# Performance work log

Hardware: AMD Instinct MI355X
Metric: run time of the kernel (lower is better)

Reference implementation:

```python
import jax, jax.numpy as jnp
import numpy as np

N_HEAD = 4
GROUPS = 32
EPS = 1e-5


def _group_norm(x, w, b):
    B, C, H, W = x.shape
    g = x.reshape(B, GROUPS, C // GROUPS, H, W)
    mu = g.mean(axis=(2, 3, 4), keepdims=True)
    var = ((g - mu) ** 2).mean(axis=(2, 3, 4), keepdims=True)
    g = (g - mu) * jax.lax.rsqrt(var + EPS)
    return g.reshape(B, C, H, W) * w[None, :, None, None] + b[None, :, None, None]


def _l2norm(x):
    # F.normalize(x, dim=-1): x / max(||x||_2, 1e-12)
    n = jnp.sqrt(jnp.sum(x * x, axis=-1, keepdims=True))
    return x / jnp.maximum(n, 1e-12)


def _masked_softmax(attn, kk):
    # topk indices -> scatter 1s -> masked softmax (faithful to torch scatter_ path)
    idx = jax.lax.top_k(attn, kk)[1]                      # [B,H,c,kk]
    mask = jax.nn.one_hot(idx, attn.shape[-1], dtype=attn.dtype).sum(-2)  # [B,H,c,c]
    return jax.nn.softmax(jnp.where(mask > 0, attn, -jnp.inf), axis=-1)


def setup_inputs() -> dict:
    key = jax.random.key(0)
    ks = jax.random.split(key, 8)
    B, C, H, W = 4, 256, 128, 128
    x = jax.random.normal(ks[0], (B, C, H, W), jnp.float32)
    gn_w = 1.0 + 0.02 * jax.random.normal(ks[1], (C,), jnp.float32)
    gn_b = 0.02 * jax.random.normal(ks[2], (C,), jnp.float32)
    w_qkv = jax.random.normal(ks[3], (3 * C, C), jnp.float32) / np.sqrt(C).astype(np.float32)
    w_dw = jax.random.normal(ks[4], (3 * C, 1, 3, 3), jnp.float32) / 3.0
    w_out = jax.random.normal(ks[5], (C, C), jnp.float32) / np.sqrt(C).astype(np.float32)
    b_out = 0.01 * jax.random.normal(ks[6], (C,), jnp.float32)
    temperature = jnp.ones((N_HEAD, 1, 1), jnp.float32)
    attn_w = jnp.full((4,), 0.2, jnp.float32)  # attn1..attn4 combine weights
    return dict(x=x, gn_w=gn_w, gn_b=gn_b, w_qkv=w_qkv, w_dw=w_dw,
                w_out=w_out, b_out=b_out, temperature=temperature, attn_w=attn_w)


def reference(x, gn_w, gn_b, w_qkv, w_dw, w_out, b_out, temperature, attn_w):
    B, C, H, W = x.shape
    c = C // N_HEAD
    xn = _group_norm(x, gn_w, gn_b)
    # 1x1 conv (no bias)
    qkv = jnp.einsum('oi,bihw->bohw', w_qkv, xn)
    # 3x3 depthwise conv, padding=1, groups=3C, no bias
    qkv = jax.lax.conv_general_dilated(
        qkv, w_dw, window_strides=(1, 1), padding=((1, 1), (1, 1)),
        feature_group_count=3 * C,
        dimension_numbers=('NCHW', 'OIHW', 'NCHW'))
    q, k, v = jnp.split(qkv, 3, axis=1)
    # b (head c) h w -> b head c (h w)
    q = q.reshape(B, N_HEAD, c, H * W)
    k = k.reshape(B, N_HEAD, c, H * W)
    v = v.reshape(B, N_HEAD, c, H * W)
    q = _l2norm(q)
    k = _l2norm(k)
    # FFT cross-correlation attention (fftshift over ALL axes, as torch default)
    q_fft = jnp.fft.fftshift(jnp.fft.rfft2(q))   # [B,H,c,HW//2+1] complex
    k_fft = jnp.fft.fftshift(jnp.fft.rfft2(k))
    attn = jnp.einsum('bhcf,bhdf->bhcd', q_fft, k_fft) * temperature  # complex [B,H,c,c]
    attn = jnp.fft.irfft2(jnp.fft.ifftshift(attn), s=(c, c))          # real [B,H,c,c]
    ks_list = [c // 2, (c * 2) // 3, (c * 3) // 4, (c * 4) // 5]
    out = None
    for i, kk in enumerate(ks_list):
        a = _masked_softmax(attn, kk)
        o = jnp.einsum('bhcd,bhds->bhcs', a, v) * attn_w[i]
        out = o if out is None else out + o
    out = out.reshape(B, C, H, W)
    out = jnp.einsum('oi,bihw->bohw', w_out, out) + b_out[None, :, None, None]
    return out
```

## Files before the change

### kernel.cpp

```cpp
#include <hip/hip_runtime.h>
#include <math.h>

#define NC 256
#define CH3 768
#define HWSZ 16384

typedef __attribute__((ext_vector_type(8))) short short8;
typedef __attribute__((ext_vector_type(4))) float f32x4;
typedef __attribute__((ext_vector_type(4))) unsigned int u32x4;

static const size_t OFF_TW1   = 0;
static const size_t OFF_TW2   = 32768;
static const size_t OFF_HM    = 65536;
static const size_t OFF_SCALE = 65600;
static const size_t OFF_SHIFT = 66624;
static const size_t OFF_PACK  = 67648;
static const size_t OFF_AW    = 182336;
static const size_t OFF_GNP   = 444480;
static const size_t SHARED_END= 446528;

static const size_t R_QKV  = 0;
static const size_t R_SCR  = 12582912;
static const size_t R_H    = 25165824;
static const size_t R_PP   = 29360128;
static const size_t R_RP   = 30408704;
static const size_t R_ATTN = 31457280;
static const size_t R_ACOMB= 31473664;
static const size_t R_PS   = 31490048;
static const size_t R_RS   = 31506432;
static const size_t R_DWP  = 31522816;
static const size_t R_SSUM = 31532032;
static const size_t R_SALT = 31532800;
static const size_t R_SSQ  = 31533568;
static const size_t RSTRIDE= 31534336;
static const size_t UROFF  = 4194304;
static const size_t UIOFF  = 8388608;

#define TDA_RH 0
#define TDA_RL 8192
#define TDA_IH 16384
#define TDA_IL 24576
#define ETA_RH 32768
#define ETA_RL 40960
#define ETA_IH 49152
#define ETA_IL 57344
#define STB_RH 65536
#define STB_RL 73728
#define STB_IH 81920
#define STB_IL 90112
#define STB_NIH 98304
#define STB_NIL 106496

#define AWQ_H 0
#define AWQ_L 98304
#define AWO_H 196608
#define AWO_L 229376

__device__ inline unsigned short b16rn(float x){
  unsigned u = __float_as_uint(x);
  return (unsigned short)((u + 0x7FFFu + ((u>>16)&1u)) >> 16);
}
__device__ inline unsigned int pk_hi(float x, float y){
  return (__float_as_uint(x)>>16) | (__float_as_uint(y) & 0xFFFF0000u);
}
__device__ inline unsigned int pk_lo(float x, float y){
  float xl = x - __uint_as_float(__float_as_uint(x) & 0xFFFF0000u);
  float yl = y - __uint_as_float(__float_as_uint(y) & 0xFFFF0000u);
  return (unsigned)b16rn(xl) | ((unsigned)b16rn(yl)<<16);
}
__device__ inline short8 ld8g(const unsigned int* p){ return *(const short8*)p; }
__device__ inline short8 ld8s(const unsigned short* p){ return *(const short8*)p; }
__device__ inline void wr_split(unsigned short* H, unsigned short* L, size_t o, float v){
  unsigned u = __float_as_uint(v);
  H[o] = (unsigned short)(u >> 16);
  L[o] = b16rn(v - __uint_as_float(u & 0xFFFF0000u));
}

__global__ __launch_bounds__(256) void init_tables_k(float* __restrict__ ws){
  int idx = blockIdx.x*256 + threadIdx.x;
  float2* tw1 = (float2*)(ws + OFF_TW1);
  float2* tw2 = (float2*)(ws + OFF_TW2);
  unsigned int* pk = (unsigned int*)(ws + OFF_PACK);
  const double P2 = 6.283185307179586476925286766559005;
  int m = idx >> 7, k = idx & 127;
  double a2 = P2 * (double)(m*k) / 16384.0;
  tw1[idx] = make_float2((float)cos(a2), (float)(-sin(a2)));
  tw2[idx] = make_float2((float)cos(a2), (float)( sin(a2)));
  if (idx < 64){
    double acc = 0.0;
    for (int v = 1; v < 32; v++) acc += sin(P2 * (double)((v*idx) & 63) / 64.0);
    ws[OFF_HM + idx] = (float)(-acc / 32.0);
  }
  if (idx < 8192){
    int r = idx >> 6, kp = idx & 63;
    int k0 = 2*kp, k1 = 2*kp+1;
    double a0 = P2 * (double)((r*k0) & 127) / 128.0;
    double a1 = P2 * (double)((r*k1) & 127) / 128.0;
    float c0 = (float)cos(a0), c1 = (float)cos(a1);
    float s0 = (float)sin(a0), s1 = (float)sin(a1);
    pk[TDA_RH + idx] = pk_hi(c0, c1);  pk[TDA_RL + idx] = pk_lo(c0, c1);
    pk[TDA_IH + idx] = pk_hi(-s0,-s1); pk[TDA_IL + idx] = pk_lo(-s0,-s1);
    pk[ETA_RH + idx] = pk_hi(c0, c1);  pk[ETA_RL + idx] = pk_lo(c0, c1);
    pk[ETA_IH + idx] = pk_hi(s0, s1);  pk[ETA_IL + idx] = pk_lo(s0, s1);
    float sr0, si0, sr1, si1;
    {
      int d0 = (r - k0) & 127, d1 = (r - k1) & 127;
      if (d0 == 0){ sr0 = 64.f; si0 = 0.f; }
      else if ((d0 & 1) == 0){ sr0 = 0.f; si0 = 0.f; }
      else { double th = 3.1415926535897932384626 * (double)d0 / 128.0;
             sr0 = 1.f; si0 = (float)(cos(th)/sin(th)); }
      if (d1 == 0){ sr1 = 64.f; si1 = 0.f; }
      else if ((d1 & 1) == 0){ sr1 = 0.f; si1 = 0.f; }
      else { double th = 3.1415926535897932384626 * (double)d1 / 128.0;
             sr1 = 1.f; si1 = (float)(cos(th)/sin(th)); }
    }
    pk[STB_RH + idx]  = pk_hi(sr0, sr1);  pk[STB_RL + idx]  = pk_lo(sr0, sr1);
    pk[STB_IH + idx]  = pk_hi(si0, si1);  pk[STB_IL + idx]  = pk_lo(si0, si1);
    pk[STB_NIH + idx] = pk_hi(-si0,-si1); pk[STB_NIL + idx] = pk_lo(-si0,-si1);
  }
}

__global__ __launch_bounds__(256) void wpack_k(const float* __restrict__ wqkv, const float* __restrict__ wout,
                                               unsigned int* __restrict__ aw){
  int id = blockIdx.x*256 + threadIdx.x;
  int row = id >> 7, kp = id & 127;
  if (row < CH3){
    float v0 = wqkv[row*256 + 2*kp], v1 = wqkv[row*256 + 2*kp + 1];
    aw[AWQ_H + row*128 + kp] = pk_hi(v0, v1);
    aw[AWQ_L + row*128 + kp] = pk_lo(v0, v1);
  } else {
    int r2 = row - CH3;
    float v0 = wout[r2*256 + 2*kp], v1 = wout[r2*256 + 2*kp + 1];
    aw[AWO_H + r2*128 + kp] = pk_hi(v0, v1);
    aw[AWO_L + r2*128 + kp] = pk_lo(v0, v1);
  }
}

__global__ __launch_bounds__(256) void gn_part_k(const float* __restrict__ x, float2* __restrict__ part){
  int id = blockIdx.x;
  const float4* p = (const float4*)(x + (size_t)id*HWSZ);
  int tid = threadIdx.x;
  float s = 0.f, sq = 0.f;
  #pragma unroll
  for (int i = 0; i < 16; i++){
    float4 v = p[tid + i*256];
    s  += v.x+v.y+v.z+v.w;
    sq += v.x*v.x+v.y*v.y+v.z*v.z+v.w*v.w;
  }
  __shared__ float r1[256], r2[256];
  r1[tid]=s; r2[tid]=sq; __syncthreads();
  for (int off=128; off; off>>=1){
    if (tid<off){ r1[tid]+=r1[tid+off]; r2[tid]+=r2[tid+off]; }
    __syncthreads();
  }
  if (tid==0) part[id] = make_float2(r1[0], r2[0]);
}
__global__ __launch_bounds__(128) void gn_fin_k(const float2* __restrict__ part, const float* __restrict__ gw,
                                                const float* __restrict__ gb, float* __restrict__ scale,
                                                float* __restrict__ shift){
  int bg = threadIdx.x;
  int b = bg >> 5, g = bg & 31;
  float s = 0.f, sq = 0.f;
  #pragma unroll
  for (int i = 0; i < 8; i++){
    float2 v = part[b*NC + g*8 + i];
    s += v.x; sq += v.y;
  }
  const float n = 8.0f*HWSZ;
  float mu = s/n, var = sq/n - mu*mu;
  float rs = rsqrtf(var + 1e-5f);
  for (int i = 0; i < 8; i++){
    int ch = g*8 + i;
    float sc = rs * gw[ch];
    scale[b*NC + ch] = sc;
    shift[b*NC + ch] = gb[ch] - mu*sc;
  }
}

__global__ __launch_bounds__(256) void packx_k(const float* __restrict__ xbase, const float* __restrict__ scale,
                                               const float* __restrict__ shift, float* __restrict__ R0,
                                               size_t rstride){
  int bz = blockIdx.z;
  const float* xb = xbase + (size_t)bz*NC*HWSZ;
  const float* sc = scale + bz*NC;
  const float* sh = shift + bz*NC;
  unsigned int* BqH = (unsigned int*)(R0 + (size_t)bz*rstride + R_H);
  unsigned int* BqL = BqH + 2097152;
  int kb = blockIdx.y;
  int n = blockIdx.x*256 + threadIdx.x;
  float v[8];
  #pragma unroll
  for (int c = 0; c < 8; c++){
    int ch = kb*8 + c;
    v[c] = xb[(size_t)ch*HWSZ + n]*sc[ch] + sh[ch];
  }
  u32x4 h, l;
  #pragma unroll
  for (int q = 0; q < 4; q++){
    h[q] = pk_hi(v[2*q], v[2*q+1]);
    l[q] = pk_lo(v[2*q], v[2*q+1]);
  }
  *(u32x4*)&BqH[((size_t)kb*HWSZ + n)*4] = h;
  *(u32x4*)&BqL[((size_t)kb*HWSZ + n)*4] = l;
}

__global__ __launch_bounds__(256) void gemm_pk(const unsigned int* __restrict__ Ah, const unsigned int* __restrict__ Al,
                                               const unsigned int* __restrict__ Bh0, const unsigned int* __restrict__ Bl0,
                                               const float* __restrict__ bias, float* __restrict__ C0,
                                               size_t bstride, size_t cstride){
  const unsigned int* Bh = Bh0 + (size_t)blockIdx.z*bstride;
  const unsigned int* Bl = Bl0 + (size_t)blockIdx.z*bstride;
  float* C = C0 + (size_t)blockIdx.z*cstride;
  int tid = threadIdx.x;
  int lane = tid & 63, wid = tid >> 6;
  int m0 = blockIdx.y*128, n0 = blockIdx.x*128;
  int wr = (wid>>1)*64, wc = (wid&1)*64;
  int lr = lane & 15, lk = lane >> 4;
  f32x4 acc[4][4] = {};
  size_t aoff[4], boff[4];
  #pragma unroll
  for (int i=0;i<4;i++) aoff[i] = (size_t)(m0 + wr + i*16 + lr)*128 + lk*4;
  #pragma unroll
  for (int j=0;j<4;j++) boff[j] = ((size_t)lk*HWSZ + n0 + wc + j*16 + lr)*4;
  short8 aH[2][4], aL[2][4], bH[2][4], bL[2][4];
  #pragma unroll
  for (int i=0;i<4;i++){ aH[0][i] = ld8g(Ah + aoff[i]); aL[0][i] = ld8g(Al + aoff[i]); }
  #pragma unroll
  for (int j=0;j<4;j++){ bH[0][j] = ld8g(Bh + boff[j]); bL[0][j] = ld8g(Bl + boff[j]); }
  #pragma unroll
  for (int kt = 0; kt < 8; kt++){
    int cur = kt & 1, nxt = cur ^ 1;
    if (kt < 7){
      size_t da = (size_t)(kt+1)*16;
      size_t db = (size_t)(kt+1)*4*HWSZ*4;
      #pragma unroll
      for (int i=0;i<4;i++){ aH[nxt][i] = ld8g(Ah + aoff[i] + da); aL[nxt][i] = ld8g(Al + aoff[i] + da); }
      #pragma unroll
      for (int j=0;j<4;j++){ bH[nxt][j] = ld8g(Bh + boff[j] + db); bL[nxt][j] = ld8g(Bl + boff[j] + db); }
    }
    #pragma unroll
    for (int i=0;i<4;i++)
      #pragma unroll
      for (int j=0;j<4;j++){
        acc[i][j] = __builtin_amdgcn_mfma_f32_16x16x32_bf16(aH[cur][i], bH[cur][j], acc[i][j], 0,0,0);
        acc[i][j] = __builtin_amdgcn_mfma_f32_16x16x32_bf16(aH[cur][i], bL[cur][j], acc[i][j], 0,0,0);
        acc[i][j] = __builtin_amdgcn_mfma_f32_16x16x32_bf16(aL[cur][i], bH[cur][j], acc[i][j], 0,0,0);
      }
  }
  #pragma unroll
  for (int i=0;i<4;i++){
    #pragma unroll
    for (int e=0;e<4;e++){
      int row = m0 + wr + i*16 + lk*4 + e;
      float bb = bias ? bias[row] : 0.0f;
      #pragma unroll
      for (int j=0;j<4;j++)
        C[(size_t)row*HWSZ + n0 + wc + j*16 + lr] = acc[i][j][e] + bb;
    }
  }
}

__global__ __launch_bounds__(256) void dwconv_tiled_k(float* __restrict__ R0, size_t rstride,
                                                      const float* __restrict__ wdw){
  float* Rb = R0 + (size_t)blockIdx.y*rstride;
  int blk = blockIdx.x;
  int ch = blk >> 2, sl = blk & 3;
  int h0 = sl*32;
  const float* in = Rb + R_SCR + (size_t)ch*HWSZ;
  float* part = Rb + R_DWP;
  float w[9];
  #pragma unroll
  for (int i=0;i<9;i++) w[i] = wdw[ch*9+i];
  __shared__ float tile[34][132];
  __shared__ float r0[256], r1[256], r2[256];
  int tid = threadIdx.x;
  #pragma unroll
  for (int i = 0; i < 5; i++){
    int id = tid + i*256;
    if (id < 1088){
      int r = id >> 5, c4 = id & 31;
      int gh = h0 - 1 + r;
      float4 v = (gh >= 0 && gh < 128) ? *(const float4*)&in[gh*128 + c4*4]
                                       : make_float4(0.f,0.f,0.f,0.f);
      *(float4*)&tile[r][c4*4] = v;
    }
  }
  __syncthreads();
  float s=0.f, sa=0.f, sq=0.f;
  #pragma unroll
  for (int it=0; it<4; it++){
    int idx = it*256 + tid;
    int lh = idx >> 5;
    int xq = idx & 31;
    int xb4 = xq*4;
    float o[4];
    #pragma unroll
    for (int e=0;e<4;e++){
      int xw = xb4 + e;
      float acc = 0.f;
      #pragma unroll
      for (int ky=0; ky<3; ky++){
        const float* tr = &tile[lh+ky][xw];
        if (xw > 0)   acc += tr[-1]*w[ky*3+0];
                      acc += tr[ 0]*w[ky*3+1];
        if (xw < 127) acc += tr[ 1]*w[ky*3+2];
      }
      o[e] = acc;
      s += acc; sq += acc*acc;
      sa += (e & 1) ? -acc : acc;
    }
    int sbase = (h0+lh)*128 + xb4;
    if (ch < 256){
      unsigned short* QHo = (unsigned short*)(Rb + R_QKV);
      unsigned short* QLo = (unsigned short*)(Rb + R_QKV + 2097152);
      size_t ro = (size_t)ch*HWSZ;
      #pragma unroll
      for (int e=0;e<4;e++){
        int sf = (16384 - (sbase+e)) & 16383;
        wr_split(QHo, QLo, ro + sf, o[e]);
      }
    } else if (ch < 512){
      unsigned short* KHo = (unsigned short*)(Rb + R_H);
      unsigned short* KLo = (unsigned short*)(Rb + R_H + 2097152);
      size_t ro = (size_t)(ch-256)*HWSZ;
      #pragma unroll
      for (int e=0;e<4;e++)
        wr_split(KHo, KLo, ro + sbase+e, o[e]);
    } else {
      *(float4*)&(Rb + R_QKV + (size_t)ch*HWSZ)[sbase] = make_float4(o[0],o[1],o[2],o[3]);
    }
  }
  r0[tid]=s; r1[tid]=sa; r2[tid]=sq; __syncthreads();
  for (int off=128; off; off>>=1){
    if (tid<off){ r0[tid]+=r0[tid+off]; r1[tid]+=r1[tid+off]; r2[tid]+=r2[tid+off]; }
    __syncthreads();
  }
  if (tid==0){ part[blk]=r0[0]; part[3072+blk]=r1[0]; part[6144+blk]=r2[0]; }
}

__global__ __launch_bounds__(256) void fft1_mfma_k(const float* __restrict__ ws, float* __restrict__ R0,
                                                   size_t rstride){
  float* Rb = R0 + (size_t)blockIdx.y*rstride;
  const unsigned short* KH = (const unsigned short*)(Rb + R_H);
  const unsigned short* KL = (const unsigned short*)(Rb + R_H + 2097152);
  unsigned short* TRH = (unsigned short*)(Rb + R_SCR);
  unsigned short* TRL = TRH + 4194304;
  unsigned short* TIH = TRL + 4194304;
  unsigned short* TIL = TIH + 4194304;
  const unsigned int* PK = (const unsigned int*)(ws + OFF_PACK);
  const float2* tw1 = (const float2*)(ws + OFF_TW1);
  __shared__ unsigned int Bth[128][20], Btl[128][20];
  int tid = threadIdx.x;
  int lane = tid & 63, wid = tid >> 6;
  int wr = (wid>>1)*64, wc = (wid&1)*64;
  int lr = lane & 15, lk = lane >> 4;
  int row = blockIdx.x;
  f32x4 aR[4][4] = {}, aI[4][4] = {};
  int bc = tid & 127, grp = tid >> 7;
  for (int kt = 0; kt < 4; kt++){
    #pragma unroll
    for (int p=0;p<8;p++){
      int kp = grp*8 + p;
      int a = kt*32 + 2*kp;
      size_t o0 = (size_t)row*HWSZ + a*128 + bc;
      Bth[bc][kp] = (unsigned)KH[o0] | ((unsigned)KH[o0+128] << 16);
      Btl[bc][kp] = (unsigned)KL[o0] | ((unsigned)KL[o0+128] << 16);
    }
    __syncthreads();
    short8 bh[4], bl[4];
    #pragma unroll
    for (int j=0;j<4;j++){
      bh[j] = *(const short8*)&Bth[wc + j*16 + lr][lk*4];
      bl[j] = *(const short8*)&Btl[wc + j*16 + lr][lk*4];
    }
    #pragma unroll
    for (int i=0;i<4;i++){
      int off = (wr + i*16 + lr)*64 + kt*16 + lk*4;
      short8 ahR = ld8g(PK + TDA_RH + off), alR = ld8g(PK + TDA_RL + off);
      short8 ahI = ld8g(PK + TDA_IH + off), alI = ld8g(PK + TDA_IL + off);
      #pragma unroll
      for (int j=0;j<4;j++){
        aR[i][j] = __builtin_amdgcn_mfma_f32_16x16x32_bf16(ahR, bh[j], aR[i][j], 0,0,0);
        aR[i][j] = __builtin_amdgcn_mfma_f32_16x16x32_bf16(ahR, bl[j], aR[i][j], 0,0,0);
        aR[i][j] = __builtin_amdgcn_mfma_f32_16x16x32_bf16(alR, bh[j], aR[i][j], 0,0,0);
        aI[i][j] = __builtin_amdgcn_mfma_f32_16x16x32_bf16(ahI, bh[j], aI[i][j], 0,0,0);
        aI[i][j] = __builtin_amdgcn_mfma_f32_16x16x32_bf16(ahI, bl[j], aI[i][j], 0,0,0);
        aI[i][j] = __builtin_amdgcn_mfma_f32_16x16x32_bf16(alI, bh[j], aI[i][j], 0,0,0);
      }
    }
    __syncthreads();
  }
  #pragma unroll
  for (int i=0;i<4;i++)
    #pragma unroll
    for (int e=0;e<4;e++){
      int m = wr + i*16 + lk*4 + e;
      #pragma unroll
      for (int j=0;j<4;j++){
        int col = wc + j*16 + lr;
        float2 t = tw1[m*128 + col];
        float r = aR[i][j][e], im = aI[i][j][e];
        float vr = r*t.x - im*t.y, vi = r*t.y + im*t.x;
        size_t o = (size_t)m*32768 + row*128 + col;
        wr_split(TRH, TRL, o, vr);
        wr_split(TIH, TIL, o, vi);
      }
    }
}

__global__ __launch_bounds__(256) void fft2_mfma_k(const float* __restrict__ ws, float* __restrict__ R0,
                                                   size_t rstride){
  float* Rb = R0 + (size_t)blockIdx.y*rstride;
  const unsigned short* TRH = (const unsigned short*)(Rb + R_SCR);
  const unsigned short* TRL = TRH + 4194304;
  const unsigned short* TIH = TRL + 4194304;
  const unsigned short* TIL = TIH + 4194304;
  unsigned short* URH = (unsigned short*)(Rb + R_QKV + UROFF);
  unsigned short* URL = URH + 4194304;
  unsigned short* UIH = (unsigned short*)(Rb + R_SCR + UIOFF);
  unsigned short* UIL = UIH + 4194304;
  const unsigned int* PK = (const unsigned int*)(ws + OFF_PACK);
  const float2* tw2 = (const float2*)(ws + OFF_TW2);
  int tid = threadIdx.x, lane = tid & 63, wid = tid >> 6;
  int row = blockIdx.x >> 1, mh = blockIdx.x & 1;
  int wr = (wid>>1)*32, wc = (wid&1)*64;
  int lr = lane & 15, lk = lane >> 4;
  f32x4 aR[2][4] = {}, aI[2][4] = {};
  size_t aoff[2];
  #pragma unroll
  for (int i=0;i<2;i++) aoff[i] = (size_t)(mh*64 + wr + i*16 + lr)*32768 + row*128 + lk*8;
  #pragma unroll
  for (int kt = 0; kt < 4; kt++){
    short8 ahR[2], alR[2], ahI[2], alI[2];
    #pragma unroll
    for (int i=0;i<2;i++){
      size_t o = aoff[i] + kt*32;
      ahR[i] = ld8s(TRH + o); alR[i] = ld8s(TRL + o);
      ahI[i] = ld8s(TIH + o); alI[i] = ld8s(TIL + o);
    }
    #pragma unroll
    for (int j=0;j<4;j++){
      int boff = (wc + j*16 + lr)*64 + kt*16 + lk*4;
      short8 bhR = ld8g(PK + STB_RH + boff), blR = ld8g(PK + STB_RL + boff);
      short8 bhI = ld8g(PK + STB_IH + boff), blI = ld8g(PK + STB_IL + boff);
      short8 bhN = ld8g(PK + STB_NIH + boff), blN = ld8g(PK + STB_NIL + boff);
      #pragma unroll
      for (int i=0;i<2;i++){
        aR[i][j] = __builtin_amdgcn_mfma_f32_16x16x32_bf16(ahR[i], bhR, aR[i][j], 0,0,0);
        aR[i][j] = __builtin_amdgcn_mfma_f32_16x16x32_bf16(ahR[i], blR, aR[i][j], 0,0,0);
        aR[i][j] = __builtin_amdgcn_mfma_f32_16x16x32_bf16(alR[i], bhR, aR[i][j], 0,0,0);
        aR[i][j] = __builtin_amdgcn_mfma_f32_16x16x32_bf16(ahI[i], bhN, aR[i][j], 0,0,0);
        aR[i][j] = __builtin_amdgcn_mfma_f32_16x16x32_bf16(ahI[i], blN, aR[i][j], 0,0,0);
        aR[i][j] = __builtin_amdgcn_mfma_f32_16x16x32_bf16(alI[i], bhN, aR[i][j], 0,0,0);
        aI[i][j] = __builtin_amdgcn_mfma_f32_16x16x32_bf16(ahR[i], bhI, aI[i][j], 0,0,0);
        aI[i][j] = __builtin_amdgcn_mfma_f32_16x16x32_bf16(ahR[i], blI, aI[i][j], 0,0,0);
        aI[i][j] = __builtin_amdgcn_mfma_f32_16x16x32_bf16(alR[i], bhI, aI[i][j], 0,0,0);
        aI[i][j] = __builtin_amdgcn_mfma_f32_16x16x32_bf16(ahI[i], bhR, aI[i][j], 0,0,0);
        aI[i][j] = __builtin_amdgcn_mfma_f32_16x16x32_bf16(ahI[i], blR, aI[i][j], 0,0,0);
        aI[i][j] = __builtin_amdgcn_mfma_f32_16x16x32_bf16(alI[i], bhR, aI[i][j], 0,0,0);
      }
    }
  }
  #pragma unroll
  for (int i=0;i<2;i++){
    int f0b = mh*64 + wr + i*16 + lk*4;
    #pragma unroll
    for (int j=0;j<4;j++){
      int r = wc + j*16 + lr;
      unsigned long long prH=0ull, prL=0ull, piH=0ull, piL=0ull;
      #pragma unroll
      for (int e=0;e<4;e++){
        float2 t = tw2[(f0b+e)*128 + r];
        float rr = aR[i][j][e], ii = aI[i][j][e];
        float ur = rr*t.x - ii*t.y, ui = rr*t.y + ii*t.x;
        unsigned uur = __float_as_uint(ur), uui = __float_as_uint(ui);
        prH |= (unsigned long long)(uur >> 16) << (16*e);
        prL |= (unsigned long long)b16rn(ur - __uint_as_float(uur & 0xFFFF0000u)) << (16*e);
        piH |= (unsigned long long)(uui >> 16) << (16*e);
        piL |= (unsigned long long)b16rn(ui - __uint_as_float(uui & 0xFFFF0000u)) << (16*e);
      }
      size_t o = (size_t)row*HWSZ + r*128 + f0b;
      *(unsigned long long*)(URH + o) = prH;
      *(unsigned long long*)(URL + o) = prL;
      *(unsigned long long*)(UIH + o) = piH;
      *(unsigned long long*)(UIL + o) = piL;
    }
  }
}

__global__ __launch_bounds__(256) void fft3_mfma_k(const float* __restrict__ ws, float* __restrict__ R0,
                                                   size_t rstride){
  float* Rb = R0 + (size_t)blockIdx.y*rstride;
  const unsigned short* URH = (const unsigned short*)(Rb + R_QKV + UROFF);
  const unsigned short* URL = URH + 4194304;
  const unsigned short* UIH = (const unsigned short*)(Rb + R_SCR + UIOFF);
  const unsigned short* UIL = UIH + 4194304;
  unsigned short* HNH = (unsigned short*)(Rb + R_SCR);
  unsigned short* HNL = HNH + 4194304;
  const unsigned int* PK = (const unsigned int*)(ws + OFF_PACK);
  int tid = threadIdx.x, lane = tid & 63, wid = tid >> 6;
  int wr = (wid>>1)*64, wc = (wid&1)*64;
  int lr = lane & 15, lk = lane >> 4;
  int row = blockIdx.x;
  f32x4 ac[4][4] = {};
  size_t boff[4];
  #pragma unroll
  for (int j=0;j<4;j++) boff[j] = (size_t)row*HWSZ + (wc + j*16 + lr)*128 + lk*8;
  #pragma unroll
  for (int kt = 0; kt < 4; kt++){
    short8 bRh[4], bRl[4], bIh[4], bIl[4];
    #pragma unroll
    for (int j=0;j<4;j++){
      bRh[j] = ld8s(URH + boff[j] + kt*32);
      bRl[j] = ld8s(URL + boff[j] + kt*32);
      bIh[j] = ld8s(UIH + boff[j] + kt*32);
      bIl[j] = ld8s(UIL + boff[j] + kt*32);
    }
    #pragma unroll
    for (int i=0;i<4;i++){
      int off = (wr + i*16 + lr)*64 + kt*16 + lk*4;
      short8 ahR = ld8g(PK + ETA_RH + off), alR = ld8g(PK + ETA_RL + off);
      short8 ahI = ld8g(PK + ETA_IH + off), alI = ld8g(PK + ETA_IL + off);
      #pragma unroll
      for (int j=0;j<4;j++){
        ac[i][j] = __builtin_amdgcn_mfma_f32_16x16x32_bf16(ahR, bIh[j], ac[i][j], 0,0,0);
        ac[i][j] = __builtin_amdgcn_mfma_f32_16x16x32_bf16(ahR, bIl[j], ac[i][j], 0,0,0);
        ac[i][j] = __builtin_amdgcn_mfma_f32_16x16x32_bf16(alR, bIh[j], ac[i][j], 0,0,0);
        ac[i][j] = __builtin_amdgcn_mfma_f32_16x16x32_bf16(ahI, bRh[j], ac[i][j], 0,0,0);
        ac[i][j] = __builtin_amdgcn_mfma_f32_16x16x32_bf16(ahI, bRl[j], ac[i][j], 0,0,0);
        ac[i][j] = __builtin_amdgcn_mfma_f32_16x16x32_bf16(alI, bRh[j], ac[i][j], 0,0,0);
      }
    }
  }
  #pragma unroll
  for (int i=0;i<4;i++)
    #pragma unroll
    for (int e=0;e<4;e++){
      int m = wr + i*16 + lk*4 + e;
      #pragma unroll
      for (int j=0;j<4;j++){
        int col = wc + j*16 + lr;
        wr_split(HNH, HNL, (size_t)row*HWSZ + m*128 + col, ac[i][j][e]);
      }
    }
}

__global__ __launch_bounds__(256) void pri3_k(float* __restrict__ R0, size_t rstride){
  float* Rb = R0 + (size_t)blockIdx.z*rstride;
  int sp = blockIdx.x, head = blockIdx.y;
  const unsigned short* QH = (const unsigned short*)(Rb + R_QKV);
  const unsigned short* QL = (const unsigned short*)(Rb + R_QKV + 2097152);
  const unsigned short* KH = (const unsigned short*)(Rb + R_H);
  const unsigned short* KL = (const unsigned short*)(Rb + R_H + 2097152);
  const unsigned short* HNH = (const unsigned short*)(Rb + R_SCR);
  const unsigned short* HNL = HNH + 4194304;
  float* Pp = Rb + R_PP;
  float* Rp = Rb + R_RP;
  int tid = threadIdx.x, lane = tid & 63, wid = tid >> 6;
  int wr = (wid>>1)*32, wc = (wid&1)*32;
  int lr = lane & 15, lk = lane >> 4;
  size_t qoff[2], koff[2];
  #pragma unroll
  for (int i=0;i<2;i++) qoff[i] = (size_t)(head*64 + wr + i*16 + lr)*HWSZ + sp*256 + lk*8;
  #pragma unroll
  for (int j=0;j<2;j++) koff[j] = (size_t)(head*64 + wc + j*16 + lr)*HWSZ + sp*256 + lk*8;
  f32x4 aP[2][2] = {}, aRi[2][2] = {};
  short8 qh[2][2], ql[2][2], k1h[2][2], k1l[2][2], k2h[2][2], k2l[2][2];
#define LDPRI(B,T) { int d = (T)*32; \
    _Pragma("unroll") \
    for (int i=0;i<2;i++){ \
      qh[B][i] = ld8s(QH + qoff[i] + d); \
      ql[B][i] = ld8s(QL + qoff[i] + d); } \
    _Pragma("unroll") \
    for (int j=0;j<2;j++){ \
      k1h[B][j] = ld8s(KH + koff[j] + d); \
      k1l[B][j] = ld8s(KL + koff[j] + d); \
      k2h[B][j] = ld8s(HNH + koff[j] + d); \
      k2l[B][j] = ld8s(HNL + koff[j] + d); } }
  LDPRI(0,0);
  #pragma unroll
  for (int kt = 0; kt < 8; kt++){
    int cur = kt & 1;
    if (kt < 7) LDPRI(cur^1, kt+1);
    #pragma unroll
    for (int i=0;i<2;i++)
      #pragma unroll
      for (int j=0;j<2;j++){
        aP[i][j]  = __builtin_amdgcn_mfma_f32_16x16x32_bf16(qh[cur][i], k1h[cur][j], aP[i][j], 0,0,0);
        aP[i][j]  = __builtin_amdgcn_mfma_f32_16x16x32_bf16(qh[cur][i], k1l[cur][j], aP[i][j], 0,0,0);
        aP[i][j]  = __builtin_amdgcn_mfma_f32_16x16x32_bf16(ql[cur][i], k1h[cur][j], aP[i][j], 0,0,0);
        aRi[i][j] = __builtin_amdgcn_mfma_f32_16x16x32_bf16(qh[cur][i], k2h[cur][j], aRi[i][j], 0,0,0);
        aRi[i][j] = __builtin_amdgcn_mfma_f32_16x16x32_bf16(qh[cur][i], k2l[cur][j], aRi[i][j], 0,0,0);
        aRi[i][j] = __builtin_amdgcn_mfma_f32_16x16x32_bf16(ql[cur][i], k2h[cur][j], aRi[i][j], 0,0,0);
      }
  }
#undef LDPRI
  size_t obase = ((size_t)(sp*4 + head)) << 12;
  #pragma unroll
  for (int i=0;i<2;i++)
    #pragma unroll
    for (int e=0;e<4;e++){
      int row = wr + i*16 + lk*4 + e;
      #pragma unroll
      for (int j=0;j<2;j++){
        int col = wc + j*16 + lr;
        size_t o = obase + (size_t)row*64 + col;
        Pp[o] = aP[i][j][e];
        Rp[o] = aRi[i][j][e];
      }
    }
}

__global__ __launch_bounds__(256) void red_k(float* __restrict__ R0, size_t rstride){
  float* Rb = R0 + (size_t)blockIdx.y*rstride;
  const float* Pp = Rb + R_PP;
  const float* Rp = Rb + R_RP;
  float* Ps = Rb + R_PS;
  float* Rs = Rb + R_RS;
  int tid = threadIdx.x;
  #pragma unroll
  for (int rep=0; rep<2; rep++){
    int g = blockIdx.x*512 + rep*256 + tid;
    int head = g >> 12, loc = g & 4095;
    float p = 0.f, ri = 0.f;
    for (int sp=0; sp<64; sp++){
      size_t o = ((size_t)(sp*4+head)<<12) + loc;
      p += Pp[o]; ri += Rp[o];
    }
    Ps[g] = p; Rs[g] = ri;
  }
  if (blockIdx.x == 0){
    const float* part = Rb + R_DWP;
    for (int ch = tid; ch < CH3; ch += 256){
      float s=0.f, sa=0.f, sq=0.f;
      #pragma unroll
      for (int sl=0; sl<4; sl++){
        s  += part[ch*4+sl];
        sa += part[3072+ch*4+sl];
        sq += part[6144+ch*4+sl];
      }
      Rb[R_SSUM+ch]=s; Rb[R_SALT+ch]=sa; Rb[R_SSQ+ch]=sq;
    }
  }
}

__global__ __launch_bounds__(256) void attn_build_k(const float* __restrict__ ws, float* __restrict__ R0,
                                                    size_t rstride, const float* __restrict__ temperature){
  float* Rb = R0 + (size_t)blockIdx.y*rstride;
  const float* Ps   = Rb + R_PS;
  const float* Rs   = Rb + R_RS;
  const float* ssum = Rb + R_SSUM;
  const float* salt = Rb + R_SALT;
  const float* ssq  = Rb + R_SSQ;
  float* attn = Rb + R_ATTN;
  const float* hmg  = ws + OFF_HM;
  __shared__ float Rn[64][65], Ril[64][65], hm[64];
  int head = blockIdx.x;
  int tid = threadIdx.x;
  if (tid < 64) hm[tid] = hmg[tid];
  for (int t=0;t<16;t++){
    int idx = tid + t*256; int c = idx>>6, d = idx&63;
    float P = Ps[head*4096 + idx], Ri = Rs[head*4096 + idx];
    int qch = head*64 + c;
    int kch = 256 + head*64 + d;
    float qs=ssum[qch], qa=salt[qch], qn=fmaxf(sqrtf(ssq[qch]), 1e-12f);
    float ks=ssum[kch], ka=salt[kch], kn=fmaxf(sqrtf(ssq[kch]), 1e-12f);
    float Rr = 0.5f*(16384.0f*P + qs*ks + qa*ka);
    float sc = 1.0f/(qn*kn);
    Rn[c][d]  = Rr*sc;
    Ril[c][d] = Ri*sc;
  }
  __syncthreads();
  float tmp2 = temperature[(head+2)&3];
  for (int t=0;t<16;t++){
    int idx = tid + t*256; int c = idx>>6, e = idx&63;
    float s = Rn[c][e];
    #pragma unroll 8
    for (int d=0; d<64; d++) s += Ril[c][d]*hm[(e-d)&63];
    attn[((size_t)head<<12) + (size_t)(c*64+e)] = s*tmp2;
  }
}

__global__ __launch_bounds__(64) void topk_k(float* __restrict__ R0, size_t rstride,
                                             const float* __restrict__ attn_w){
  float* Rb = R0 + (size_t)blockIdx.y*rstride;
  const float* attn = Rb + R_ATTN;
  float* Acomb = Rb + R_ACOMB;
  int blk = blockIdx.x;
  int tid = threadIdx.x;
  __shared__ float row[64];
  float v = attn[(size_t)blk*64 + tid];
  row[tid] = v;
  __syncthreads();
  int rank = 0; float vmax = -1e30f;
  for (int l=0;l<64;l++){
    float w = row[l];
    if (w > v || (w == v && l < tid)) rank++;
    vmax = fmaxf(vmax, w);
  }
  float e = expf(v - vmax);
  const int kks[4] = {32,42,48,51};
  float denom[4];
  #pragma unroll
  for (int i=0;i<4;i++){
    float x = (rank < kks[i]) ? e : 0.0f;
    #pragma unroll
    for (int off=32; off; off>>=1) x += __shfl_xor(x, off);
    denom[i] = x;
  }
  float wgt = 0.f;
  #pragma unroll
  for (int i=0;i<4;i++) if (rank < kks[i]) wgt += attn_w[i] / denom[i];
  Acomb[(size_t)blk*64 + tid] = e * wgt;
}

__global__ __launch_bounds__(256) void av_k(float* __restrict__ R0, size_t rstride){
  float* Rb = R0 + (size_t)blockIdx.z*rstride;
  const float* Acomb = Rb + R_ACOMB;
  unsigned int* BqH = (unsigned int*)(Rb + R_H);
  unsigned int* BqL = BqH + 2097152;
  int head = blockIdx.y;
  int n0 = blockIdx.x*64;
  const float* Vb = Rb + R_QKV + (size_t)(512 + head*64)*HWSZ;
  __shared__ float As[64][65], Bs[16][65];
  int tid=threadIdx.x, tx=tid&15, ty=tid>>4;
  for (int t=0;t<16;t++){ int idx=tid+t*256; As[idx>>6][idx&63] = Acomb[((size_t)head<<12)+idx]; }
  __syncthreads();
  float acc[4][4]={};
  for (int k0=0;k0<64;k0+=16){
    #pragma unroll
    for (int i=0;i<4;i++){ int id=tid+i*256; int nn=id&63, k=id>>6;
      Bs[k][nn] = Vb[(size_t)(k0+k)*HWSZ + n0+nn]; }
    __syncthreads();
    #pragma unroll
    for (int k=0;k<16;k++){
      float a[4], bv[4];
      #pragma unroll
      for (int i=0;i<4;i++) a[i]=As[ty*4+i][k0+k];
      #pragma unroll
      for (int j=0;j<4;j++) bv[j]=Bs[k][tx*4+j];
      #pragma unroll
      for (int i=0;i<4;i++)
        #pragma unroll
        for (int j=0;j<4;j++) acc[i][j] += a[i]*bv[j];
    }
    __syncthreads();
  }
  int kpa = head*32 + ty*2;
  int kba = kpa >> 2, qa = kpa & 3;
  int kpb = kpa + 1;
  int kbb = kpb >> 2, qb = kpb & 3;
  #pragma unroll
  for (int j=0;j<4;j++){
    int n = n0 + tx*4 + j;
    BqH[((size_t)kba*HWSZ + n)*4 + qa] = pk_hi(acc[0][j], acc[1][j]);
    BqL[((size_t)kba*HWSZ + n)*4 + qa] = pk_lo(acc[0][j], acc[1][j]);
    BqH[((size_t)kbb*HWSZ + n)*4 + qb] = pk_hi(acc[2][j], acc[3][j]);
    BqL[((size_t)kbb*HWSZ + n)*4 + qb] = pk_lo(acc[2][j], acc[3][j]);
  }
}

extern "C" void kernel_launch(void* const* d_in, const int* in_sizes, int n_in,
                              void* d_out, int out_size, void* d_ws, size_t ws_size,
                              hipStream_t stream) {
  const float* x     = (const float*)d_in[0];
  const float* gn_w  = (const float*)d_in[1];
  const float* gn_b  = (const float*)d_in[2];
  const float* w_qkv = (const float*)d_in[3];
  const float* w_dw  = (const float*)d_in[4];
  const float* w_out = (const float*)d_in[5];
  const float* b_out = (const float*)d_in[6];
  const float* temperature = (const float*)d_in[7];
  const float* attn_w = (const float*)d_in[8];
  float* out = (float*)d_out;
  float* ws  = (float*)d_ws;
  unsigned int* AW = (unsigned int*)(ws + OFF_AW);
  float* R0 = ws + SHARED_END;
  const size_t CHW = (size_t)NC*HWSZ;

  size_t need2 = (SHARED_END + 2*RSTRIDE)*sizeof(float);
  size_t need4 = (SHARED_END + 4*RSTRIDE)*sizeof(float);
  int zb = (ws_size >= need4) ? 4 : (ws_size >= need2) ? 2 : 1;

  init_tables_k<<<64,256,0,stream>>>(ws);
  wpack_k<<<512,256,0,stream>>>(w_qkv, w_out, AW);
  gn_part_k<<<1024,256,0,stream>>>(x, (float2*)(ws+OFF_GNP));
  gn_fin_k<<<1,128,0,stream>>>((const float2*)(ws+OFF_GNP), gn_w, gn_b,
                               ws+OFF_SCALE, ws+OFF_SHIFT);

  for (int b0 = 0; b0 < 4; b0 += zb){
    packx_k<<<dim3(64,32,zb),256,0,stream>>>(x + (size_t)b0*CHW, ws+OFF_SCALE+b0*NC,
                                             ws+OFF_SHIFT+b0*NC, R0, RSTRIDE);
    gemm_pk<<<dim3(128,6,zb),256,0,stream>>>(AW+AWQ_H, AW+AWQ_L,
                                             (unsigned int*)(R0+R_H), (unsigned int*)(R0+R_H)+2097152,
                                             nullptr, R0+R_SCR, RSTRIDE, RSTRIDE);
    dwconv_tiled_k<<<dim3(3072,zb),256,0,stream>>>(R0, RSTRIDE, w_dw);
    fft1_mfma_k<<<dim3(256,zb),256,0,stream>>>(ws, R0, RSTRIDE);
    fft2_mfma_k<<<dim3(512,zb),256,0,stream>>>(ws, R0, RSTRIDE);
    fft3_mfma_k<<<dim3(256,zb),256,0,stream>>>(ws, R0, RSTRIDE);
    pri3_k<<<dim3(64,4,zb),256,0,stream>>>(R0, RSTRIDE);
    red_k<<<dim3(32,zb),256,0,stream>>>(R0, RSTRIDE);
    attn_build_k<<<dim3(4,zb),256,0,stream>>>(ws, R0, RSTRIDE, temperature);
    topk_k<<<dim3(256,zb),64,0,stream>>>(R0, RSTRIDE, attn_w);
    av_k<<<dim3(256,4,zb),256,0,stream>>>(R0, RSTRIDE);
    gemm_pk<<<dim3(128,2,zb),256,0,stream>>>(AW+AWO_H, AW+AWO_L,
                                             (unsigned int*)(R0+R_H), (unsigned int*)(R0+R_H)+2097152,
                                             b_out, out + (size_t)b0*CHW, RSTRIDE, CHW);
  }
}
```

Measured before the change: 906.5 us.

## Fuse FFT stages two and three through shared-memory staging of intermediates

Merges the second and third FFT matrix-multiply stages into one kernel per row d. The intermediate twiddled spectrum is kept in LDS (split into bf16 hi/lo planes) instead of being written to and re-read from global memory, and the second GEMM accumulates over two 64-wide K halves. This removes one launch and a large global round trip of bf16 hi/lo buffers. In exchange it uses about 72KB of LDS per block, which limits occupancy, and it halves the grid size of stage two, which also serialises its work.

```diff
diff --git a/kernel.cpp b/kernel.cpp
--- a/kernel.cpp
+++ b/kernel.cpp
@@ -33,8 +33,7 @@
 static const size_t R_SALT = 31532800;
 static const size_t R_SSQ  = 31533568;
 static const size_t RSTRIDE= 31534336;
-static const size_t UROFF  = 4194304;
-static const size_t UIOFF  = 8388608;
+static const size_t HOFF   = 4194304;
 
 #define TDA_RH 0
 #define TDA_RL 8192
@@ -55,6 +54,8 @@
 #define AWQ_L 98304
 #define AWO_H 196608
 #define AWO_L 229376
+
+#define USTR 72
 
 __device__ inline unsigned short b16rn(float x){
   unsigned u = __float_as_uint(x);
@@ -408,127 +409,114 @@
     }
 }
 
-__global__ __launch_bounds__(256) void fft2_mfma_k(const float* __restrict__ ws, float* __restrict__ R0,
-                                                   size_t rstride){
+__global__ __launch_bounds__(256) void fft23_mfma_k(const float* __restrict__ ws, float* __restrict__ R0,
+                                                    size_t rstride){
   float* Rb = R0 + (size_t)blockIdx.y*rstride;
   const unsigned short* TRH = (const unsigned short*)(Rb + R_SCR);
   const unsigned short* TRL = TRH + 4194304;
   const unsigned short* TIH = TRL + 4194304;
   const unsigned short* TIL = TIH + 4194304;
-  unsigned short* URH = (unsigned short*)(Rb + R_QKV + UROFF);
-  unsigned short* URL = URH + 4194304;
-  unsigned short* UIH = (unsigned short*)(Rb + R_SCR + UIOFF);
-  unsigned short* UIL = UIH + 4194304;
+  unsigned short* HNH = (unsigned short*)(Rb + R_QKV + HOFF);
+  unsigned short* HNL = HNH + 4194304;
   const unsigned int* PK = (const unsigned int*)(ws + OFF_PACK);
   const float2* tw2 = (const float2*)(ws + OFF_TW2);
+  __shared__ unsigned short U4[4][128][USTR];
   int tid = threadIdx.x, lane = tid & 63, wid = tid >> 6;
-  int row = blockIdx.x >> 1, mh = blockIdx.x & 1;
-  int wr = (wid>>1)*32, wc = (wid&1)*64;
   int lr = lane & 15, lk = lane >> 4;
-  f32x4 aR[2][4] = {}, aI[2][4] = {};
-  size_t aoff[2];
-  #pragma unroll
-  for (int i=0;i<2;i++) aoff[i] = (size_t)(mh*64 + wr + i*16 + lr)*32768 + row*128 + lk*8;
-  #pragma unroll
-  for (int kt = 0; kt < 4; kt++){
-    short8 ahR[2], alR[2], ahI[2], alI[2];
+  int d = blockIdx.x;
+  int wr2 = (wid>>1)*64, wc2 = (wid&1)*64;
+  f32x4 ac[4][4] = {};
+  int wr1 = (wid>>1)*32, wc1 = (wid&1)*64;
+
+  for (int mh = 0; mh < 2; mh++){
+    f32x4 aR[2][4] = {}, aI[2][4] = {};
+    size_t aoff[2];
+    #pragma unroll
+    for (int i=0;i<2;i++) aoff[i] = (size_t)(mh*64 + wr1 + i*16 + lr)*32768 + (size_t)d*128 + lk*8;
+    #pragma unroll
+    for (int kt = 0; kt < 4; kt++){
+      short8 ahR[2], alR[2], ahI[2], alI[2];
+      #pragma unroll
+      for (int i=0;i<2;i++){
+        size_t o = aoff[i] + kt*32;
+        ahR[i] = ld8s(TRH + o); alR[i] = ld8s(TRL + o);
+        ahI[i] = ld8s(TIH + o); alI[i] = ld8s(TIL + o);
+      }
+      #pragma unroll
+      for (int j=0;j<4;j++){
+        int boff = (wc1 + j*16 + lr)*64 + kt*16 + lk*4;
+        short8 bhR = ld8g(PK + STB_RH + boff), blR = ld8g(PK + STB_RL + boff);
+        short8 bhI = ld8g(PK + STB_IH + boff), blI = ld8g(PK + STB_IL + boff);
+        short8 bhN = ld8g(PK + STB_NIH + boff), blN = ld8g(PK + STB_NIL + boff);
+        #pragma unroll
+        for (int i=0;i<2;i++){
+          aR[i][j] = __builtin_amdgcn_mfma_f32_16x16x32_bf16(ahR[i], bhR, aR[i][j], 0,0,0);
+          aR[i][j] = __builtin_amdgcn_mfma_f32_16x16x32_bf16(ahR[i], blR, aR[i][j], 0,0,0);
+          aR[i][j] = __builtin_amdgcn_mfma_f32_16x16x32_bf16(alR[i], bhR, aR[i][j], 0,0,0);
+          aR[i][j] = __builtin_amdgcn_mfma_f32_16x16x32_bf16(ahI[i], bhN, aR[i][j], 0,0,0);
+          aR[i][j] = __builtin_amdgcn_mfma_f32_16x16x32_bf16(ahI[i], blN, aR[i][j], 0,0,0);
+          aR[i][j] = __builtin_amdgcn_mfma_f32_16x16x32_bf16(alI[i], bhN, aR[i][j], 0,0,0);
+          aI[i][j] = __builtin_amdgcn_mfma_f32_16x16x32_bf16(ahR[i], bhI, aI[i][j], 0,0,0);
+          aI[i][j] = __builtin_amdgcn_mfma_f32_16x16x32_bf16(ahR[i], blI, aI[i][j], 0,0,0);
+          aI[i][j] = __builtin_amdgcn_mfma_f32_16x16x32_bf16(alR[i], bhI, aI[i][j], 0,0,0);
+          aI[i][j] = __builtin_amdgcn_mfma_f32_16x16x32_bf16(ahI[i], bhR, aI[i][j], 0,0,0);
+          aI[i][j] = __builtin_amdgcn_mfma_f32_16x16x32_bf16(ahI[i], blR, aI[i][j], 0,0,0);
+          aI[i][j] = __builtin_amdgcn_mfma_f32_16x16x32_bf16(alI[i], bhR, aI[i][j], 0,0,0);
+        }
+      }
+    }
+    if (mh) __syncthreads();
     #pragma unroll
     for (int i=0;i<2;i++){
-      size_t o = aoff[i] + kt*32;
-      ahR[i] = ld8s(TRH + o); alR[i] = ld8s(TRL + o);
-      ahI[i] = ld8s(TIH + o); alI[i] = ld8s(TIL + o);
-    }
-    #pragma unroll
-    for (int j=0;j<4;j++){
-      int boff = (wc + j*16 + lr)*64 + kt*16 + lk*4;
-      short8 bhR = ld8g(PK + STB_RH + boff), blR = ld8g(PK + STB_RL + boff);
-      short8 bhI = ld8g(PK + STB_IH + boff), blI = ld8g(PK + STB_IL + boff);
-      short8 bhN = ld8g(PK + STB_NIH + boff), blN = ld8g(PK + STB_NIL + boff);
-      #pragma unroll
-      for (int i=0;i<2;i++){
-        aR[i][j] = __builtin_amdgcn_mfma_f32_16x16x32_bf16(ahR[i], bhR, aR[i][j], 0,0,0);
-        aR[i][j] = __builtin_amdgcn_mfma_f32_16x16x32_bf16(ahR[i], blR, aR[i][j], 0,0,0);
-        aR[i][j] = __builtin_amdgcn_mfma_f32_16x16x32_bf16(alR[i], bhR, aR[i][j], 0,0,0);
-        aR[i][j] = __builtin_amdgcn_mfma_f32_16x16x32_bf16(ahI[i], bhN, aR[i][j], 0,0,0);
-        aR[i][j] = __builtin_amdgcn_mfma_f32_16x16x32_bf16(ahI[i], blN, aR[i][j], 0,0,0);
-        aR[i][j] = __builtin_amdgcn_mfma_f32_16x16x32_bf16(alI[i], bhN, aR[i][j], 0,0,0);
-        aI[i][j] = __builtin_amdgcn_mfma_f32_16x16x32_bf16(ahR[i], bhI, aI[i][j], 0,0,0);
-        aI[i][j] = __builtin_amdgcn_mfma_f32_16x16x32_bf16(ahR[i], blI, aI[i][j], 0,0,0);
-        aI[i][j] = __builtin_amdgcn_mfma_f32_16x16x32_bf16(alR[i], bhI, aI[i][j], 0,0,0);
-        aI[i][j] = __builtin_amdgcn_mfma_f32_16x16x32_bf16(ahI[i], bhR, aI[i][j], 0,0,0);
-        aI[i][j] = __builtin_amdgcn_mfma_f32_16x16x32_bf16(ahI[i], blR, aI[i][j], 0,0,0);
-        aI[i][j] = __builtin_amdgcn_mfma_f32_16x16x32_bf16(alI[i], bhR, aI[i][j], 0,0,0);
-      }
-    }
-  }
-  #pragma unroll
-  for (int i=0;i<2;i++){
-    int f0b = mh*64 + wr + i*16 + lk*4;
-    #pragma unroll
-    for (int j=0;j<4;j++){
-      int r = wc + j*16 + lr;
-      unsigned long long prH=0ull, prL=0ull, piH=0ull, piL=0ull;
-      #pragma unroll
-      for (int e=0;e<4;e++){
-        float2 t = tw2[(f0b+e)*128 + r];
-        float rr = aR[i][j][e], ii = aI[i][j][e];
-        float ur = rr*t.x - ii*t.y, ui = rr*t.y + ii*t.x;
-        unsigned uur = __float_as_uint(ur), uui = __float_as_uint(ui);
-        prH |= (unsigned long long)(uur >> 16) << (16*e);
-        prL |= (unsigned long long)b16rn(ur - __uint_as_float(uur & 0xFFFF0000u)) << (16*e);
-        piH |= (unsigned long long)(uui >> 16) << (16*e);
-        piL |= (unsigned long long)b16rn(ui - __uint_as_float(uui & 0xFFFF0000u)) << (16*e);
-      }
-      size_t o = (size_t)row*HWSZ + r*128 + f0b;
-      *(unsigned long long*)(URH + o) = prH;
-      *(unsigned long long*)(URL + o) = prL;
-      *(unsigned long long*)(UIH + o) = piH;
-      *(unsigned long long*)(UIL + o) = piL;
-    }
-  }
-}
-
-__global__ __launch_bounds__(256) void fft3_mfma_k(const float* __restrict__ ws, float* __restrict__ R0,
-                                                   size_t rstride){
-  float* Rb = R0 + (size_t)blockIdx.y*rstride;
-  const unsigned short* URH = (const unsigned short*)(Rb + R_QKV + UROFF);
-  const unsigned short* URL = URH + 4194304;
-  const unsigned short* UIH = (const unsigned short*)(Rb + R_SCR + UIOFF);
-  const unsigned short* UIL = UIH + 4194304;
-  unsigned short* HNH = (unsigned short*)(Rb + R_SCR);
-  unsigned short* HNL = HNH + 4194304;
-  const unsigned int* PK = (const unsigned int*)(ws + OFF_PACK);
-  int tid = threadIdx.x, lane = tid & 63, wid = tid >> 6;
-  int wr = (wid>>1)*64, wc = (wid&1)*64;
-  int lr = lane & 15, lk = lane >> 4;
-  int row = blockIdx.x;
-  f32x4 ac[4][4] = {};
-  size_t boff[4];
-  #pragma unroll
-  for (int j=0;j<4;j++) boff[j] = (size_t)row*HWSZ + (wc + j*16 + lr)*128 + lk*8;
-  #pragma unroll
-  for (int kt = 0; kt < 4; kt++){
-    short8 bRh[4], bRl[4], bIh[4], bIl[4];
-    #pragma unroll
-    for (int j=0;j<4;j++){
-      bRh[j] = ld8s(URH + boff[j] + kt*32);
-      bRl[j] = ld8s(URL + boff[j] + kt*32);
-      bIh[j] = ld8s(UIH + boff[j] + kt*32);
-      bIl[j] = ld8s(UIL + boff[j] + kt*32);
-    }
-    #pragma unroll
-    for (int i=0;i<4;i++){
-      int off = (wr + i*16 + lr)*64 + kt*16 + lk*4;
-      short8 ahR = ld8g(PK + ETA_RH + off), alR = ld8g(PK + ETA_RL + off);
-      short8 ahI = ld8g(PK + ETA_IH + off), alI = ld8g(PK + ETA_IL + off);
+      int f0l = wr1 + i*16 + lk*4;
       #pragma unroll
       for (int j=0;j<4;j++){
-        ac[i][j] = __builtin_amdgcn_mfma_f32_16x16x32_bf16(ahR, bIh[j], ac[i][j], 0,0,0);
-        ac[i][j] = __builtin_amdgcn_mfma_f32_16x16x32_bf16(ahR, bIl[j], ac[i][j], 0,0,0);
-        ac[i][j] = __builtin_amdgcn_mfma_f32_16x16x32_bf16(alR, bIh[j], ac[i][j], 0,0,0);
-        ac[i][j] = __builtin_amdgcn_mfma_f32_16x16x32_bf16(ahI, bRh[j], ac[i][j], 0,0,0);
-        ac[i][j] = __builtin_amdgcn_mfma_f32_16x16x32_bf16(ahI, bRl[j], ac[i][j], 0,0,0);
-        ac[i][j] = __builtin_amdgcn_mfma_f32_16x16x32_bf16(alI, bRh[j], ac[i][j], 0,0,0);
+        int r = wc1 + j*16 + lr;
+        unsigned long long prH=0ull, prL=0ull, piH=0ull, piL=0ull;
+        #pragma unroll
+        for (int e=0;e<4;e++){
+          float2 t = tw2[(mh*64 + f0l + e)*128 + r];
+          float rr = aR[i][j][e], ii = aI[i][j][e];
+          float ur = rr*t.x - ii*t.y, ui = rr*t.y + ii*t.x;
+          unsigned uur = __float_as_uint(ur), uui = __float_as_uint(ui);
+          prH |= (unsigned long long)(uur >> 16) << (16*e);
+          prL |= (unsigned long long)b16rn(ur - __uint_as_float(uur & 0xFFFF0000u)) << (16*e);
+          piH |= (unsigned long long)(uui >> 16) << (16*e);
+          piL |= (unsigned long long)b16rn(ui - __uint_as_float(uui & 0xFFFF0000u)) << (16*e);
+        }
+        *(unsigned long long*)&U4[0][r][f0l] = prH;
+        *(unsigned long long*)&U4[1][r][f0l] = prL;
+        *(unsigned long long*)&U4[2][r][f0l] = piH;
+        *(unsigned long long*)&U4[3][r][f0l] = piL;
+      }
+    }
+    __syncthreads();
+    #pragma unroll
+    for (int kt = 0; kt < 2; kt++){
+      short8 bRh[4], bRl[4], bIh[4], bIl[4];
+      #pragma unroll
+      for (int j=0;j<4;j++){
+        int r = wc2 + j*16 + lr;
+        int ko = kt*32 + lk*8;
+        bRh[j] = *(const short8*)&U4[0][r][ko];
+        bRl[j] = *(const short8*)&U4[1][r][ko];
+        bIh[j] = *(const short8*)&U4[2][r][ko];
+        bIl[j] = *(const short8*)&U4[3][r][ko];
+      }
+      #pragma unroll
+      for (int i=0;i<4;i++){
+        int off = (wr2 + i*16 + lr)*64 + mh*32 + kt*16 + lk*4;
+        short8 ahR = ld8g(PK + ETA_RH + off), alR = ld8g(PK + ETA_RL + off);
+        short8 ahI = ld8g(PK + ETA_IH + off), alI = ld8g(PK + ETA_IL + off);
+        #pragma unroll
+        for (int j=0;j<4;j++){
+          ac[i][j] = __builtin_amdgcn_mfma_f32_16x16x32_bf16(ahR, bIh[j], ac[i][j], 0,0,0);
+          ac[i][j] = __builtin_amdgcn_mfma_f32_16x16x32_bf16(ahR, bIl[j], ac[i][j], 0,0,0);
+          ac[i][j] = __builtin_amdgcn_mfma_f32_16x16x32_bf16(alR, bIh[j], ac[i][j], 0,0,0);
+          ac[i][j] = __builtin_amdgcn_mfma_f32_16x16x32_bf16(ahI, bRh[j], ac[i][j], 0,0,0);
+          ac[i][j] = __builtin_amdgcn_mfma_f32_16x16x32_bf16(ahI, bRl[j], ac[i][j], 0,0,0);
+          ac[i][j] = __builtin_amdgcn_mfma_f32_16x16x32_bf16(alI, bRh[j], ac[i][j], 0,0,0);
+        }
       }
     }
   }
@@ -536,11 +524,11 @@
   for (int i=0;i<4;i++)
     #pragma unroll
     for (int e=0;e<4;e++){
-      int m = wr + i*16 + lk*4 + e;
+      int m = wr2 + i*16 + lk*4 + e;
       #pragma unroll
       for (int j=0;j<4;j++){
-        int col = wc + j*16 + lr;
-        wr_split(HNH, HNL, (size_t)row*HWSZ + m*128 + col, ac[i][j][e]);
+        int col = wc2 + j*16 + lr;
+        wr_split(HNH, HNL, (size_t)d*HWSZ + m*128 + col, ac[i][j][e]);
       }
     }
 }
@@ -552,7 +540,7 @@
   const unsigned short* QL = (const unsigned short*)(Rb + R_QKV + 2097152);
   const unsigned short* KH = (const unsigned short*)(Rb + R_H);
   const unsigned short* KL = (const unsigned short*)(Rb + R_H + 2097152);
-  const unsigned short* HNH = (const unsigned short*)(Rb + R_SCR);
+  const unsigned short* HNH = (const unsigned short*)(Rb + R_QKV + HOFF);
   const unsigned short* HNL = HNH + 4194304;
   float* Pp = Rb + R_PP;
   float* Rp = Rb + R_RP;
@@ -796,8 +784,7 @@
                                              nullptr, R0+R_SCR, RSTRIDE, RSTRIDE);
     dwconv_tiled_k<<<dim3(3072,zb),256,0,stream>>>(R0, RSTRIDE, w_dw);
     fft1_mfma_k<<<dim3(256,zb),256,0,stream>>>(ws, R0, RSTRIDE);
-    fft2_mfma_k<<<dim3(512,zb),256,0,stream>>>(ws, R0, RSTRIDE);
-    fft3_mfma_k<<<dim3(256,zb),256,0,stream>>>(ws, R0, RSTRIDE);
+    fft23_mfma_k<<<dim3(256,zb),256,0,stream>>>(ws, R0, RSTRIDE);
     pri3_k<<<dim3(64,4,zb),256,0,stream>>>(R0, RSTRIDE);
     red_k<<<dim3(32,zb),256,0,stream>>>(R0, RSTRIDE);
     attn_build_k<<<dim3(4,zb),256,0,stream>>>(ws, R0, RSTRIDE, temperature);
```

Result: slower. 954.7 us (+5.3%).
